# Optimization experiments

Hardware: AMD Instinct MI355X
Metric: run time of the kernel (lower is better)

## Reference

```python
import jax, jax.numpy as jnp
import numpy as np

L = 5          # num_layer
H = 32         # num_heads (feature dim)
G = 32         # n_graph
NN = 256       # n_node per graph
KB = 8         # adjacency band half-width
N = G * (2 * (KB * NN - KB * (KB + 1) // 2))   # 128768 angle-graph nodes
E = N * 16                                      # 2060288 angle-graph edges
NRBF = 20
BN_EPS = 1e-5
GAMMA = 10.0


def _band_adj():
    i = np.arange(NN)
    d = np.abs(i[:, None] - i[None, :])
    a = (d <= KB) & (d > 0)
    return jnp.asarray(np.broadcast_to(a, (G, NN, NN)).copy())


def setup_inputs() -> dict:
    key = jax.random.key(0)
    ks = jax.random.split(key, 10)
    adj = _band_adj()
    x_mask = jnp.ones((G, NN), dtype=bool)
    x_3d = jax.random.uniform(ks[0], (N, 1), minval=0.8, maxval=1.8)
    edge_attr_3d = jax.random.uniform(ks[1], (E, 1), minval=0.0, maxval=float(np.pi))
    edge_index = jax.random.randint(ks[2], (2, E), 0, N)
    s1 = 1.0 / np.sqrt(NRBF)
    sH = 1.0 / np.sqrt(H)
    s2H = 1.0 / np.sqrt(2 * H)
    return {
        "x_3d": x_3d, "edge_attr_3d": edge_attr_3d,
        "edge_index": edge_index, "adj": adj, "x_mask": x_mask,
        "w_len": jax.random.normal(ks[3], (NRBF, H)) * s1, "b_len": jnp.zeros(H),
        "w_ang": jax.random.normal(ks[4], (NRBF, H)) * s1, "b_ang": jnp.zeros(H),
        "w1": jax.random.normal(ks[5], (L, H, 2 * H)) * sH, "b1": jnp.zeros((L, 2 * H)),
        "bn1_g": jnp.ones((L, 2 * H)), "bn1_b": jnp.zeros((L, 2 * H)),
        "w2": jax.random.normal(ks[6], (L, 2 * H, H)) * s2H, "b2": jnp.zeros((L, H)),
        "eps_gin": jnp.zeros(L),
        "bn_g": jnp.ones((L, H)), "bn_b": jnp.zeros((L, H)),
        "ln_g": jnp.ones(H), "ln_b": jnp.zeros(H),
    }


def _bn(h, g, b):
    # BatchNorm1d in training mode (batch statistics)
    m = jnp.mean(h, axis=0)
    v = jnp.var(h, axis=0)
    return (h - m) * jax.lax.rsqrt(v + BN_EPS) * g + b


def _rbf(x, centers):
    # x: [M,1] -> [M, NRBF]
    return jnp.exp(-GAMMA * (x - centers) ** 2)


def _forward(x_3d, edge_attr_3d, edge_index, adj,
             w_len, b_len, w_ang, b_ang,
             w1, b1, bn1_g, bn1_b, w2, b2, eps_gin, bn_g, bn_b, ln_g, ln_b):
    cen_len = jnp.arange(NRBF, dtype=x_3d.dtype) * 0.1           # bond length RBF centers
    cen_ang = jnp.linspace(0.0, np.pi, NRBF).astype(x_3d.dtype)  # bond angle RBF centers
    x = _rbf(x_3d, cen_len) @ w_len + b_len                      # [N,H]
    ea = _rbf(edge_attr_3d, cen_ang) @ w_ang + b_ang             # [E,H]
    src, dst = edge_index[0], edge_index[1]

    h = x
    for l in range(L):
        # GINConvBondAngle: message = relu(x_j + edge_attr); aggr = add
        msg = jax.nn.relu(h[src] + ea)                           # [E,H]
        agg = jax.ops.segment_sum(msg, dst, num_segments=N)      # [N,H]
        z = (1.0 + eps_gin[l]) * h + agg
        z = _bn(z @ w1[l] + b1[l], bn1_g[l], bn1_b[l])           # mlp Linear+BN
        z = jax.nn.relu(z) @ w2[l] + b2[l]                       # mlp ReLU+Linear
        h = _bn(z, bn_g[l], bn_b[l])                             # outer batch norm
        if l != L - 1:
            h = jax.nn.relu(h)
        # dropout p=0 -> identity; residual=False; JK='last'

    mu = jnp.mean(h, axis=-1, keepdims=True)
    var = jnp.var(h, axis=-1, keepdims=True)
    nr = (h - mu) * jax.lax.rsqrt(var + BN_EPS) * ln_g + ln_b    # LayerNorm, [N,H]

    # masked dense scatter into [G*NN*NN, H]
    eye = jnp.eye(NN, dtype=bool)
    mask = (adj & ~eye).reshape(-1)                              # exactly N Trues
    pos = jnp.cumsum(mask) - 1                                   # row in nr for each True
    out = jnp.where(mask[:, None], nr[jnp.clip(pos, 0, N - 1)], 0.0)
    return out.reshape(G, NN, NN, H).transpose(0, 3, 1, 2)       # [G,H,NN,NN]


def reference(x_3d, edge_attr_3d, edge_index, adj, x_mask,
              w_len, b_len, w_ang, b_ang,
              w1, b1, bn1_g, bn1_b, w2, b2, eps_gin, bn_g, bn_b, ln_g, ln_b):
    return _forward(x_3d, edge_attr_3d, edge_index, adj,
                    w_len, b_len, w_ang, b_ang,
                    w1, b1, bn1_g, bn1_b, w2, b2, eps_gin, bn_g, bn_b, ln_g, ln_b)
```

## Files before the change

### kernel.cpp

```cpp
#include <hip/hip_runtime.h>
#include <hip/hip_bf16.h>
#include <hip/hip_fp16.h>

#define HH 32
#define HH2 64
#define NRBF_ 20
#define NL 5
#define NNN 256
#define KBW 8
#define PGN 4024
#define TTAB 4096
constexpr int NNODE = 128768;
constexpr int NEDGE = 2060288;
constexpr float BNEPS = 1e-5f;
constexpr float PI_F = 3.14159265358979323846f;

#define EMB_BLKS (NNODE * HH / 256)
#define TAB_BLKS (TTAB * HH / 256)
#define HIST_BLKS (NEDGE / 256)

__global__ void __launch_bounds__(256) k_prep(const float* __restrict__ x3d,
                                              const float* __restrict__ wlen,
                                              const float* __restrict__ blen,
                                              const float* __restrict__ wang,
                                              const float* __restrict__ bang,
                                              const int* __restrict__ dst,
                                              __half* __restrict__ hbuf,
                                              __half* __restrict__ tab,
                                              int* __restrict__ counts) {
  int b = blockIdx.x;
  int t = threadIdx.x;
  if (b < EMB_BLKS) {
    __shared__ float wl[NRBF_ * HH];
    __shared__ float bl[HH];
    for (int j = t; j < NRBF_ * HH; j += 256) wl[j] = wlen[j];
    if (t < HH) bl[t] = blen[t];
    __syncthreads();
    int idx = b * 256 + t;
    int n = idx >> 5, c = idx & 31;
    float x = x3d[n];
    float acc = bl[c];
#pragma unroll
    for (int k = 0; k < NRBF_; ++k) {
      float d = x - 0.1f * (float)k;
      acc = fmaf(__expf(-10.f * d * d), wl[k * HH + c], acc);
    }
    hbuf[idx] = __float2half(acc);
  } else if (b < EMB_BLKS + TAB_BLKS) {
    __shared__ float wa[NRBF_ * HH];
    __shared__ float ba[HH];
    for (int j = t; j < NRBF_ * HH; j += 256) wa[j] = wang[j];
    if (t < HH) ba[t] = bang[t];
    __syncthreads();
    int idx = (b - EMB_BLKS) * 256 + t;
    int row = idx >> 5, c = idx & 31;
    float ang = (float)row * (PI_F / (float)(TTAB - 1));
    const float step = PI_F / 19.f;
    float acc = ba[c];
#pragma unroll
    for (int k = 0; k < NRBF_; ++k) {
      float d = ang - step * (float)k;
      acc = fmaf(__expf(-10.f * d * d), wa[k * HH + c], acc);
    }
    tab[row * HH + c] = __float2half(acc);
  } else {
    int e = (b - EMB_BLKS - TAB_BLKS) * 256 + t;
    atomicAdd(&counts[dst[e]], 1);
  }
}

__global__ void __launch_bounds__(256) k_scan1(const int* __restrict__ counts, int* __restrict__ bsum) {
  __shared__ int sd[256];
  int t = threadIdx.x;
  sd[t] = counts[blockIdx.x * 256 + t];
  __syncthreads();
  for (int s = 128; s > 0; s >>= 1) { if (t < s) sd[t] += sd[t + s]; __syncthreads(); }
  if (t == 0) bsum[blockIdx.x] = sd[0];
}

__global__ void __launch_bounds__(512) k_scan2(const int* __restrict__ bsum, int* __restrict__ boff) {
  __shared__ int sd[512];
  int t = threadIdx.x;
  int v = (t < 503) ? bsum[t] : 0;
  sd[t] = v;
  __syncthreads();
  for (int off = 1; off < 512; off <<= 1) {
    int x = (t >= off) ? sd[t - off] : 0;
    __syncthreads();
    sd[t] += x;
    __syncthreads();
  }
  if (t < 503) boff[t] = sd[t] - v;
}

__global__ void __launch_bounds__(256) k_scan3(const int* __restrict__ counts, const int* __restrict__ boff,
                                               int* __restrict__ rowptr, int* __restrict__ cursor) {
  __shared__ int sd[256];
  int t = threadIdx.x;
  int i = blockIdx.x * 256 + t;
  int v = counts[i];
  sd[t] = v;
  __syncthreads();
  for (int off = 1; off < 256; off <<= 1) {
    int x = (t >= off) ? sd[t - off] : 0;
    __syncthreads();
    sd[t] += x;
    __syncthreads();
  }
  int excl = sd[t] - v + boff[blockIdx.x];
  rowptr[i] = excl;
  cursor[i] = excl;
  if (i == NNODE - 1) rowptr[NNODE] = excl + v;
}

__global__ void __launch_bounds__(256) k_scatter(const int* __restrict__ srcA,
                                                 const int* __restrict__ dstA,
                                                 const float* __restrict__ eattr,
                                                 int* __restrict__ cursor,
                                                 unsigned int* __restrict__ pk) {
  const float angsc = (float)(TTAB - 1) / PI_F;
  int bid = blockIdx.x;
  int x = bid & 7;
  int j = bid >> 3;
  int lo = x * (NNODE / 8);
  int hi = lo + (NNODE / 8);
  int e0 = j * 2048 + threadIdx.x;
#pragma unroll
  for (int k = 0; k < 8; ++k) {
    int e = e0 + k * 256;
    int d = dstA[e];
    if (d >= lo && d < hi) {
      int pos = atomicAdd(&cursor[d], 1);
      unsigned int idx = min((unsigned int)fmaf(eattr[e], angsc, 0.5f), (unsigned int)(TTAB - 1));
      pk[pos] = (unsigned int)srcA[e] | (idx << 17);
    }
  }
}

__global__ void __launch_bounds__(256) k_layerA(const __half* __restrict__ hbuf,
                                                const int* __restrict__ rowptr,
                                                const unsigned int* __restrict__ pk,
                                                const __half* __restrict__ tab,
                                                const float* __restrict__ statsC,
                                                const float* __restrict__ bng,
                                                const float* __restrict__ bnb,
                                                const float* __restrict__ w1g,
                                                const float* __restrict__ b1g,
                                                const float* __restrict__ epsg,
                                                __half* __restrict__ y1buf,
                                                float* __restrict__ statsA,
                                                int l, int relu) {
  __shared__ float w1s[HH * HH2];
  __shared__ float b1s[HH2];
  __shared__ float affs[HH], affsh[HH];
  __shared__ float tb[32][HH + 1];
  __shared__ float ps[HH2], pq[HH2];
  int t = threadIdx.x;
  const float* w1l = w1g + l * HH * HH2;
  for (int j = t; j < HH * HH2; j += 256) w1s[j] = w1l[j];
  if (t < HH2) { b1s[t] = b1g[l * HH2 + t]; ps[t] = 0.f; pq[t] = 0.f; }
  if (t < HH) {
    if (l == 0) { affs[t] = 1.f; affsh[t] = 0.f; }
    else {
      float sum = statsC[(l - 1) * 64 + t], sq = statsC[(l - 1) * 64 + 32 + t];
      float mean = sum / (float)NNODE;
      float var = fmaxf(sq / (float)NNODE - mean * mean, 0.f);
      float s = bng[(l - 1) * HH + t] * rsqrtf(var + BNEPS);
      affs[t] = s; affsh[t] = bnb[(l - 1) * HH + t] - mean * s;
    }
  }
  int g = t >> 3, c = t & 7;
  int c4 = c * 4, c8 = c * 8;
  float epsv = 1.f + epsg[l];
  float lo = relu ? 0.f : -3.4e38f;
  float sA0 = 0.f, sA1 = 0.f, sA2 = 0.f, sA3 = 0.f, sA4 = 0.f, sA5 = 0.f, sA6 = 0.f, sA7 = 0.f;
  float sQ0 = 0.f, sQ1 = 0.f, sQ2 = 0.f, sQ3 = 0.f, sQ4 = 0.f, sQ5 = 0.f, sQ6 = 0.f, sQ7 = 0.f;
  __syncthreads();
  float sc0 = affs[c4], sh0 = affsh[c4];
  float sc1 = affs[c4 + 1], sh1 = affsh[c4 + 1];
  float sc2 = affs[c4 + 2], sh2 = affsh[c4 + 2];
  float sc3 = affs[c4 + 3], sh3 = affsh[c4 + 3];
  int stride = gridDim.x * 32;
  int iters = (NNODE + stride - 1) / stride;
  int n = blockIdx.x * 32 + g;
  for (int it = 0; it < iters; ++it, n += stride) {
    bool val = n < NNODE;
    if (val) {
      int p0 = rowptr[n], p1 = rowptr[n + 1];
      uint2 HN = *(const uint2*)&hbuf[n * HH + c4];
      float2 hn01 = __half22float2(*(__half2*)&HN.x);
      float2 hn23 = __half22float2(*(__half2*)&HN.y);
      float a0 = 0.f, a1 = 0.f, a2 = 0.f, a3 = 0.f;
      for (int p = p0; p < p1; p += 8) {
        unsigned int qv[8];
        float okf[8];
        uint2 Hv[8], Ev[8];
#pragma unroll
        for (int i = 0; i < 8; ++i) {
          int pi = p + i;
          bool ok = pi < p1;
          okf[i] = ok ? 1.f : 0.f;
          qv[i] = __builtin_nontemporal_load(&pk[ok ? pi : p0]);
        }
#pragma unroll
        for (int i = 0; i < 8; ++i) {
          Hv[i] = *(const uint2*)&hbuf[(qv[i] & 0x1FFFF) * HH + c4];
          Ev[i] = *(const uint2*)&tab[(qv[i] >> 17) * HH + c4];
        }
#pragma unroll
        for (int i = 0; i < 8; ++i) {
          float2 f01 = __half22float2(*(__half2*)&Hv[i].x);
          float2 f23 = __half22float2(*(__half2*)&Hv[i].y);
          float2 e01 = __half22float2(*(__half2*)&Ev[i].x);
          float2 e23 = __half22float2(*(__half2*)&Ev[i].y);
          a0 += okf[i] * fmaxf(fmaxf(fmaf(f01.x, sc0, sh0), lo) + e01.x, 0.f);
          a1 += okf[i] * fmaxf(fmaxf(fmaf(f01.y, sc1, sh1), lo) + e01.y, 0.f);
          a2 += okf[i] * fmaxf(fmaxf(fmaf(f23.x, sc2, sh2), lo) + e23.x, 0.f);
          a3 += okf[i] * fmaxf(fmaxf(fmaf(f23.y, sc3, sh3), lo) + e23.y, 0.f);
        }
      }
      tb[g][c4]     = fmaf(epsv, fmaxf(fmaf(hn01.x, sc0, sh0), lo), a0);
      tb[g][c4 + 1] = fmaf(epsv, fmaxf(fmaf(hn01.y, sc1, sh1), lo), a1);
      tb[g][c4 + 2] = fmaf(epsv, fmaxf(fmaf(hn23.x, sc2, sh2), lo), a2);
      tb[g][c4 + 3] = fmaf(epsv, fmaxf(fmaf(hn23.y, sc3, sh3), lo), a3);
    }
    __builtin_amdgcn_wave_barrier();
    if (val) {
      float y0 = b1s[c8], y1 = b1s[c8 + 1], y2 = b1s[c8 + 2], y3 = b1s[c8 + 3];
      float y4 = b1s[c8 + 4], y5 = b1s[c8 + 5], y6 = b1s[c8 + 6], y7 = b1s[c8 + 7];
#pragma unroll
      for (int k = 0; k < HH; ++k) {
        float tk = tb[g][k];
        const float* wr = &w1s[k * HH2 + c8];
        y0 = fmaf(tk, wr[0], y0); y1 = fmaf(tk, wr[1], y1);
        y2 = fmaf(tk, wr[2], y2); y3 = fmaf(tk, wr[3], y3);
        y4 = fmaf(tk, wr[4], y4); y5 = fmaf(tk, wr[5], y5);
        y6 = fmaf(tk, wr[6], y6); y7 = fmaf(tk, wr[7], y7);
      }
      __half2 h01 = __floats2half2_rn(y0, y1);
      __half2 h23 = __floats2half2_rn(y2, y3);
      __half2 h45 = __floats2half2_rn(y4, y5);
      __half2 h67 = __floats2half2_rn(y6, y7);
      uint4 pack;
      pack.x = *(unsigned int*)&h01; pack.y = *(unsigned int*)&h23;
      pack.z = *(unsigned int*)&h45; pack.w = *(unsigned int*)&h67;
      *(uint4*)&y1buf[n * HH2 + c8] = pack;
      float2 z01 = __half22float2(h01), z23 = __half22float2(h23);
      float2 z45 = __half22float2(h45), z67 = __half22float2(h67);
      sA0 += z01.x; sQ0 += z01.x * z01.x; sA1 += z01.y; sQ1 += z01.y * z01.y;
      sA2 += z23.x; sQ2 += z23.x * z23.x; sA3 += z23.y; sQ3 += z23.y * z23.y;
      sA4 += z45.x; sQ4 += z45.x * z45.x; sA5 += z45.y; sQ5 += z45.y * z45.y;
      sA6 += z67.x; sQ6 += z67.x * z67.x; sA7 += z67.y; sQ7 += z67.y * z67.y;
    }
    __builtin_amdgcn_wave_barrier();
  }
#define RED(v) v += __shfl_xor(v, 8); v += __shfl_xor(v, 16); v += __shfl_xor(v, 32);
  RED(sA0) RED(sA1) RED(sA2) RED(sA3) RED(sA4) RED(sA5) RED(sA6) RED(sA7)
  RED(sQ0) RED(sQ1) RED(sQ2) RED(sQ3) RED(sQ4) RED(sQ5) RED(sQ6) RED(sQ7)
#undef RED
  if ((t & 63) < 8) {
    atomicAdd(&ps[c8], sA0); atomicAdd(&ps[c8 + 1], sA1);
    atomicAdd(&ps[c8 + 2], sA2); atomicAdd(&ps[c8 + 3], sA3);
    atomicAdd(&ps[c8 + 4], sA4); atomicAdd(&ps[c8 + 5], sA5);
    atomicAdd(&ps[c8 + 6], sA6); atomicAdd(&ps[c8 + 7], sA7);
    atomicAdd(&pq[c8], sQ0); atomicAdd(&pq[c8 + 1], sQ1);
    atomicAdd(&pq[c8 + 2], sQ2); atomicAdd(&pq[c8 + 3], sQ3);
    atomicAdd(&pq[c8 + 4], sQ4); atomicAdd(&pq[c8 + 5], sQ5);
    atomicAdd(&pq[c8 + 6], sQ6); atomicAdd(&pq[c8 + 7], sQ7);
  }
  __syncthreads();
  if (t < HH2) {
    atomicAdd(&statsA[l * 128 + t], ps[t]);
    atomicAdd(&statsA[l * 128 + 64 + t], pq[t]);
  }
}

__global__ void __launch_bounds__(256) k_layerC(const __half* __restrict__ y1buf,
                                                const float* __restrict__ statsA,
                                                const float* __restrict__ g1,
                                                const float* __restrict__ bb1,
                                                const float* __restrict__ w2g,
                                                const float* __restrict__ b2g,
                                                __half* __restrict__ hbuf,
                                                float* __restrict__ statsC, int l) {
  __shared__ float w2s[HH2 * HH];
  __shared__ float b2s[HH];
  __shared__ float a1s[HH2], a1sh[HH2];
  __shared__ float ab[32][HH2 + 2];
  __shared__ float ps[HH], pq[HH];
  int t = threadIdx.x;
  const float* w2l = w2g + l * HH2 * HH;
  for (int j = t; j < HH2 * HH; j += 256) w2s[j] = w2l[j];
  if (t < HH) { b2s[t] = b2g[l * HH + t]; ps[t] = 0.f; pq[t] = 0.f; }
  if (t < HH2) {
    float sum = statsA[l * 128 + t], sq = statsA[l * 128 + 64 + t];
    float mean = sum / (float)NNODE;
    float var = fmaxf(sq / (float)NNODE - mean * mean, 0.f);
    float s = g1[l * HH2 + t] * rsqrtf(var + BNEPS);
    a1s[t] = s; a1sh[t] = bb1[l * HH2 + t] - mean * s;
  }
  int g = t >> 3, c = t & 7;
  int c8 = c * 8, c4 = c * 4;
  float sa0 = 0.f, sq0 = 0.f, sa1 = 0.f, sq1 = 0.f;
  float sa2 = 0.f, sq2 = 0.f, sa3 = 0.f, sq3 = 0.f;
  __syncthreads();
  int stride = gridDim.x * 32;
  int iters = (NNODE + stride - 1) / stride;
  int n = blockIdx.x * 32 + g;
  for (int it = 0; it < iters; ++it, n += stride) {
    bool val = n < NNODE;
    if (val) {
      uint4 Y = *(const uint4*)&y1buf[n * HH2 + c8];
      float2 y01 = __half22float2(*(__half2*)&Y.x);
      float2 y23 = __half22float2(*(__half2*)&Y.y);
      float2 y45 = __half22float2(*(__half2*)&Y.z);
      float2 y67 = __half22float2(*(__half2*)&Y.w);
      ab[g][c8]     = fmaxf(fmaf(y01.x, a1s[c8],     a1sh[c8]),     0.f);
      ab[g][c8 + 1] = fmaxf(fmaf(y01.y, a1s[c8 + 1], a1sh[c8 + 1]), 0.f);
      ab[g][c8 + 2] = fmaxf(fmaf(y23.x, a1s[c8 + 2], a1sh[c8 + 2]), 0.f);
      ab[g][c8 + 3] = fmaxf(fmaf(y23.y, a1s[c8 + 3], a1sh[c8 + 3]), 0.f);
      ab[g][c8 + 4] = fmaxf(fmaf(y45.x, a1s[c8 + 4], a1sh[c8 + 4]), 0.f);
      ab[g][c8 + 5] = fmaxf(fmaf(y45.y, a1s[c8 + 5], a1sh[c8 + 5]), 0.f);
      ab[g][c8 + 6] = fmaxf(fmaf(y67.x, a1s[c8 + 6], a1sh[c8 + 6]), 0.f);
      ab[g][c8 + 7] = fmaxf(fmaf(y67.y, a1s[c8 + 7], a1sh[c8 + 7]), 0.f);
    }
    __builtin_amdgcn_wave_barrier();
    if (val) {
      float z0 = b2s[c4], z1 = b2s[c4 + 1], z2 = b2s[c4 + 2], z3 = b2s[c4 + 3];
#pragma unroll
      for (int k = 0; k < HH2; ++k) {
        float ak = ab[g][k];
        const float* wr = &w2s[k * HH + c4];
        z0 = fmaf(ak, wr[0], z0); z1 = fmaf(ak, wr[1], z1);
        z2 = fmaf(ak, wr[2], z2); z3 = fmaf(ak, wr[3], z3);
      }
      __half2 zh01 = __floats2half2_rn(z0, z1);
      __half2 zh23 = __floats2half2_rn(z2, z3);
      uint2 pack;
      pack.x = *(unsigned int*)&zh01; pack.y = *(unsigned int*)&zh23;
      *(uint2*)&hbuf[n * HH + c4] = pack;
      float2 zf01 = __half22float2(zh01), zf23 = __half22float2(zh23);
      sa0 += zf01.x; sq0 += zf01.x * zf01.x;
      sa1 += zf01.y; sq1 += zf01.y * zf01.y;
      sa2 += zf23.x; sq2 += zf23.x * zf23.x;
      sa3 += zf23.y; sq3 += zf23.y * zf23.y;
    }
    __builtin_amdgcn_wave_barrier();
  }
#define RED(v) v += __shfl_xor(v, 8); v += __shfl_xor(v, 16); v += __shfl_xor(v, 32);
  RED(sa0) RED(sa1) RED(sa2) RED(sa3)
  RED(sq0) RED(sq1) RED(sq2) RED(sq3)
#undef RED
  if ((t & 63) < 8) {
    atomicAdd(&ps[c4], sa0); atomicAdd(&ps[c4 + 1], sa1);
    atomicAdd(&ps[c4 + 2], sa2); atomicAdd(&ps[c4 + 3], sa3);
    atomicAdd(&pq[c4], sq0); atomicAdd(&pq[c4 + 1], sq1);
    atomicAdd(&pq[c4 + 2], sq2); atomicAdd(&pq[c4 + 3], sq3);
  }
  __syncthreads();
  if (t < HH) atomicAdd(&statsC[l * 64 + t], ps[t]);
  else if (t < HH2) atomicAdd(&statsC[l * 64 + t], pq[t - HH]);
}

__global__ void __launch_bounds__(256) k_output(const __half* __restrict__ hbuf,
                                                const float* __restrict__ statsC,
                                                const float* __restrict__ bng,
                                                const float* __restrict__ bnb,
                                                const float* __restrict__ lng,
                                                const float* __restrict__ lnb,
                                                float* __restrict__ out) {
  __shared__ float nrb[16 * 33];
  __shared__ float affs[HH], affsh[HH];
  int t = threadIdx.x;
  if (t < HH) {
    float sum = statsC[(NL - 1) * 64 + t], sq = statsC[(NL - 1) * 64 + 32 + t];
    float mean = sum / (float)NNODE;
    float var = fmaxf(sq / (float)NNODE - mean * mean, 0.f);
    float s = bng[(NL - 1) * HH + t] * rsqrtf(var + BNEPS);
    affs[t] = s; affsh[t] = bnb[(NL - 1) * HH + t] - mean * s;
  }
  __syncthreads();
  int gi = blockIdx.x;
  int g = gi >> 8, i = gi & 255;
  int jlo = (i - KBW > 0) ? i - KBW : 0;
  int jhi = (i + KBW < NNN - 1) ? i + KBW : NNN - 1;
  int cnt = jhi - jlo;
  int Ai = (i <= 8) ? i * (i - 1) / 2 : 28 + 8 * (i - 8);
  int Bi = (i <= 248) ? 8 * i : 2012 - (256 - i) * (255 - i) / 2;
  int nb = g * PGN + Ai + Bi;
  int r = t >> 5, c = t & 31;
  float sc = affs[c], sh = affsh[c];
  float lg = lng[c], lb = lnb[c];
  for (int rr = r; rr < cnt; rr += 8) {
    float v = fmaf(__half2float(hbuf[(nb + rr) * HH + c]), sc, sh);
    float s = v;
#pragma unroll
    for (int off = 16; off > 0; off >>= 1) s += __shfl_xor(s, off, 32);
    float mean = s * (1.f / 32.f);
    float d = v - mean;
    float q = d * d;
#pragma unroll
    for (int off = 16; off > 0; off >>= 1) q += __shfl_xor(q, off, 32);
    float var = q * (1.f / 32.f);
    nrb[rr * 33 + c] = d * rsqrtf(var + BNEPS) * lg + lb;
  }
  __syncthreads();
  int j = t;
  bool valid = (j >= jlo) & (j <= jhi) & (j != i);
  int rr = j - jlo - ((j > i) ? 1 : 0);
  rr = (rr < 0) ? 0 : ((rr > 15) ? 15 : rr);
  size_t ob = (((size_t)g * HH) * NNN + i) * NNN + j;
#pragma unroll
  for (int h = 0; h < HH; ++h) {
    float val = valid ? nrb[rr * 33 + h] : 0.f;
    __builtin_nontemporal_store(val, &out[ob + (size_t)h * NNN * NNN]);
  }
}

extern "C" void kernel_launch(void* const* d_in, const int* in_sizes, int n_in,
                              void* d_out, int out_size, void* d_ws, size_t ws_size,
                              hipStream_t stream) {
  (void)in_sizes; (void)n_in;
  const float* x3d   = (const float*)d_in[0];
  const float* eattr = (const float*)d_in[1];
  const int*   eidx  = (const int*)d_in[2];
  const float* wlen = (const float*)d_in[5];
  const float* blen = (const float*)d_in[6];
  const float* wang = (const float*)d_in[7];
  const float* bang = (const float*)d_in[8];
  const float* w1g  = (const float*)d_in[9];
  const float* b1g  = (const float*)d_in[10];
  const float* g1   = (const float*)d_in[11];
  const float* bb1  = (const float*)d_in[12];
  const float* w2g  = (const float*)d_in[13];
  const float* b2g  = (const float*)d_in[14];
  const float* epsg = (const float*)d_in[15];
  const float* bng  = (const float*)d_in[16];
  const float* bnb  = (const float*)d_in[17];
  const float* lng  = (const float*)d_in[18];
  const float* lnb  = (const float*)d_in[19];
  float* out = (float*)d_out;

  char* ws = (char*)d_ws;
  size_t off = 0;
  auto alloc = [&](size_t bytes) {
    void* p = ws + off;
    off += (bytes + 255) & ~(size_t)255;
    return p;
  };
  unsigned int* pk  = (unsigned int*)alloc((size_t)NEDGE * 4);
  int*   rowptr     = (int*)alloc((size_t)(NNODE + 1) * 4);
  int*   counts     = (int*)alloc((size_t)NNODE * 4);
  float* statsA     = (float*)alloc((NL * 128 + NL * 64) * 4);
  float* statsC     = statsA + NL * 128;
  int*   cursor     = (int*)alloc((size_t)NNODE * 4);
  __half* hbuf      = (__half*)alloc((size_t)NNODE * HH * 2);
  __half* y1buf     = (__half*)alloc((size_t)NNODE * HH2 * 2);
  __half* tab       = (__half*)alloc((size_t)TTAB * HH * 2);
  int*   bsum       = (int*)alloc(503 * 4);
  int*   boff       = (int*)alloc(503 * 4);

  if (off > ws_size) {
    hipMemsetAsync(d_out, 0x7F, (size_t)out_size * 4, stream);
    return;
  }

  hipMemsetAsync(counts, 0, (size_t)NNODE * 4 + (NL * 128 + NL * 64) * 4, stream);

  k_prep<<<EMB_BLKS + TAB_BLKS + HIST_BLKS, 256, 0, stream>>>(x3d, wlen, blen, wang, bang,
                                                              eidx + NEDGE, hbuf, tab, counts);
  k_scan1<<<NNODE / 256, 256, 0, stream>>>(counts, bsum);
  k_scan2<<<1, 512, 0, stream>>>(bsum, boff);
  k_scan3<<<NNODE / 256, 256, 0, stream>>>(counts, boff, rowptr, cursor);
  k_scatter<<<8048, 256, 0, stream>>>(eidx, eidx + NEDGE, eattr, cursor, pk);

  for (int l = 0; l < NL; ++l) {
    int relu = l >= 1 ? 1 : 0;
    k_layerA<<<2048, 256, 0, stream>>>(hbuf, rowptr, pk, tab, statsC, bng, bnb,
                                       w1g, b1g, epsg, y1buf, statsA, l, relu);
    k_layerC<<<2048, 256, 0, stream>>>(y1buf, statsA, g1, bb1, w2g, b2g, hbuf, statsC, l);
  }

  k_output<<<NNN * 32, 256, 0, stream>>>(hbuf, statsC, bng, bnb, lng, lnb, out);
}
```

Baseline: 945.7 us.

## Use packed fp16 math, shuffled index loads, and a peeled tail in edge aggregation

The per-edge message loop in the layer-A kernel now computes the affine, ReLU and edge-add in packed half2 arithmetic and accumulates through fdot2 into fp32. Each of the 8 lanes of a node group loads one packed edge index and shares it with the others through a width-8 shuffle, so the eight redundant index loads per lane are gone. Full batches of 8 edges run without masking, and only a peeled tail batch is masked. The intermediate math now runs in fp16, which costs precision, and the non-ReLU lower clamp changes to -60000 to stay inside the half range.

Measured after the change: 930.2 us. No clear change (-1.6%).

```diff
diff --git a/kernel.cpp b/kernel.cpp
--- a/kernel.cpp
+++ b/kernel.cpp
@@ -19,6 +19,28 @@
 #define TAB_BLKS (TTAB * HH / 256)
 #define HIST_BLKS (NEDGE / 256)
 
+typedef _Float16 h2v __attribute__((ext_vector_type(2)));
+
+union U32H2 { unsigned int u; h2v v; };
+
+__device__ __forceinline__ h2v u2h(unsigned int u) { U32H2 x; x.u = u; return x.v; }
+
+__device__ __forceinline__ h2v hmax2v(h2v a, h2v b) {
+#if __has_builtin(__builtin_elementwise_max)
+  return __builtin_elementwise_max(a, b);
+#else
+  h2v r; r.x = a.x > b.x ? a.x : b.x; r.y = a.y > b.y ? a.y : b.y; return r;
+#endif
+}
+
+__device__ __forceinline__ float fdot2f(h2v a, h2v b, float c) {
+#if __has_builtin(__builtin_amdgcn_fdot2)
+  return __builtin_amdgcn_fdot2(a, b, c, false);
+#else
+  return fmaf((float)a.x, (float)b.x, fmaf((float)a.y, (float)b.y, c));
+#endif
+}
+
 __global__ void __launch_bounds__(256) k_prep(const float* __restrict__ x3d,
                                               const float* __restrict__ wlen,
                                               const float* __restrict__ blen,
@@ -134,6 +156,44 @@
       unsigned int idx = min((unsigned int)fmaf(eattr[e], angsc, 0.5f), (unsigned int)(TTAB - 1));
       pk[pos] = (unsigned int)srcA[e] | (idx << 17);
     }
+  }
+}
+
+template<bool MASK>
+__device__ __forceinline__ void edge_batch(const __half* __restrict__ hbuf,
+                                           const __half* __restrict__ tab,
+                                           unsigned int myq, int p, int p1, int c4,
+                                           h2v sc01, h2v sh01,
+                                           h2v sc23, h2v sh23, h2v lo2,
+                                           float& a0, float& a1, float& a2, float& a3) {
+  unsigned int qv[8];
+  uint2 Hv[8], Ev[8];
+#pragma unroll
+  for (int i = 0; i < 8; ++i) qv[i] = (unsigned int)__shfl((int)myq, i, 8);
+#pragma unroll
+  for (int i = 0; i < 8; ++i) {
+    Hv[i] = *(const uint2*)&hbuf[(qv[i] & 0x1FFFF) * HH + c4];
+    Ev[i] = *(const uint2*)&tab[(qv[i] >> 17) * HH + c4];
+  }
+  const h2v selA = {(_Float16)1.f, (_Float16)0.f};
+  const h2v selB = {(_Float16)0.f, (_Float16)1.f};
+  const h2v zz   = {(_Float16)0.f, (_Float16)0.f};
+#pragma unroll
+  for (int i = 0; i < 8; ++i) {
+    h2v mkA = selA, mkB = selB;
+    if (MASK) {
+      bool ok = (p + i) < p1;
+      mkA = ok ? selA : zz;
+      mkB = ok ? selB : zz;
+    }
+    h2v h01 = u2h(Hv[i].x), h23 = u2h(Hv[i].y);
+    h2v e01 = u2h(Ev[i].x), e23 = u2h(Ev[i].y);
+    h2v m01 = hmax2v(hmax2v(h01 * sc01 + sh01, lo2) + e01, zz);
+    h2v m23 = hmax2v(hmax2v(h23 * sc23 + sh23, lo2) + e23, zz);
+    a0 = fdot2f(m01, mkA, a0);
+    a1 = fdot2f(m01, mkB, a1);
+    a2 = fdot2f(m23, mkA, a2);
+    a3 = fdot2f(m23, mkB, a3);
   }
 }
 
@@ -172,14 +232,17 @@
   int g = t >> 3, c = t & 7;
   int c4 = c * 4, c8 = c * 8;
   float epsv = 1.f + epsg[l];
-  float lo = relu ? 0.f : -3.4e38f;
+  float lof = relu ? 0.f : -60000.f;
   float sA0 = 0.f, sA1 = 0.f, sA2 = 0.f, sA3 = 0.f, sA4 = 0.f, sA5 = 0.f, sA6 = 0.f, sA7 = 0.f;
   float sQ0 = 0.f, sQ1 = 0.f, sQ2 = 0.f, sQ3 = 0.f, sQ4 = 0.f, sQ5 = 0.f, sQ6 = 0.f, sQ7 = 0.f;
   __syncthreads();
-  float sc0 = affs[c4], sh0 = affsh[c4];
-  float sc1 = affs[c4 + 1], sh1 = affsh[c4 + 1];
-  float sc2 = affs[c4 + 2], sh2 = affsh[c4 + 2];
-  float sc3 = affs[c4 + 3], sh3 = affsh[c4 + 3];
+  float sc0f = affs[c4], sh0f = affsh[c4];
+  float sc1f = affs[c4 + 1], sh1f = affsh[c4 + 1];
+  float sc2f = affs[c4 + 2], sh2f = affsh[c4 + 2];
+  float sc3f = affs[c4 + 3], sh3f = affsh[c4 + 3];
+  h2v sc01 = {(_Float16)sc0f, (_Float16)sc1f}, sh01 = {(_Float16)sh0f, (_Float16)sh1f};
+  h2v sc23 = {(_Float16)sc2f, (_Float16)sc3f}, sh23 = {(_Float16)sh2f, (_Float16)sh3f};
+  h2v lo2 = {(_Float16)lof, (_Float16)lof};
   int stride = gridDim.x * 32;
   int iters = (NNODE + stride - 1) / stride;
   int n = blockIdx.x * 32 + g;
@@ -191,38 +254,20 @@
       float2 hn01 = __half22float2(*(__half2*)&HN.x);
       float2 hn23 = __half22float2(*(__half2*)&HN.y);
       float a0 = 0.f, a1 = 0.f, a2 = 0.f, a3 = 0.f;
-      for (int p = p0; p < p1; p += 8) {
-        unsigned int qv[8];
-        float okf[8];
-        uint2 Hv[8], Ev[8];
-#pragma unroll
-        for (int i = 0; i < 8; ++i) {
-          int pi = p + i;
-          bool ok = pi < p1;
-          okf[i] = ok ? 1.f : 0.f;
-          qv[i] = __builtin_nontemporal_load(&pk[ok ? pi : p0]);
-        }
-#pragma unroll
-        for (int i = 0; i < 8; ++i) {
-          Hv[i] = *(const uint2*)&hbuf[(qv[i] & 0x1FFFF) * HH + c4];
-          Ev[i] = *(const uint2*)&tab[(qv[i] >> 17) * HH + c4];
-        }
-#pragma unroll
-        for (int i = 0; i < 8; ++i) {
-          float2 f01 = __half22float2(*(__half2*)&Hv[i].x);
-          float2 f23 = __half22float2(*(__half2*)&Hv[i].y);
-          float2 e01 = __half22float2(*(__half2*)&Ev[i].x);
-          float2 e23 = __half22float2(*(__half2*)&Ev[i].y);
-          a0 += okf[i] * fmaxf(fmaxf(fmaf(f01.x, sc0, sh0), lo) + e01.x, 0.f);
-          a1 += okf[i] * fmaxf(fmaxf(fmaf(f01.y, sc1, sh1), lo) + e01.y, 0.f);
-          a2 += okf[i] * fmaxf(fmaxf(fmaf(f23.x, sc2, sh2), lo) + e23.x, 0.f);
-          a3 += okf[i] * fmaxf(fmaxf(fmaf(f23.y, sc3, sh3), lo) + e23.y, 0.f);
-        }
+      int p = p0;
+      for (; p + 8 <= p1; p += 8) {
+        unsigned int myq = __builtin_nontemporal_load(&pk[p + c]);
+        edge_batch<false>(hbuf, tab, myq, p, p1, c4, sc01, sh01, sc23, sh23, lo2, a0, a1, a2, a3);
       }
-      tb[g][c4]     = fmaf(epsv, fmaxf(fmaf(hn01.x, sc0, sh0), lo), a0);
-      tb[g][c4 + 1] = fmaf(epsv, fmaxf(fmaf(hn01.y, sc1, sh1), lo), a1);
-      tb[g][c4 + 2] = fmaf(epsv, fmaxf(fmaf(hn23.x, sc2, sh2), lo), a2);
-      tb[g][c4 + 3] = fmaf(epsv, fmaxf(fmaf(hn23.y, sc3, sh3), lo), a3);
+      if (p < p1) {
+        int pidx = p + c;
+        unsigned int myq = __builtin_nontemporal_load(&pk[pidx < p1 ? pidx : p]);
+        edge_batch<true>(hbuf, tab, myq, p, p1, c4, sc01, sh01, sc23, sh23, lo2, a0, a1, a2, a3);
+      }
+      tb[g][c4]     = fmaf(epsv, fmaxf(fmaf(hn01.x, sc0f, sh0f), lof), a0);
+      tb[g][c4 + 1] = fmaf(epsv, fmaxf(fmaf(hn01.y, sc1f, sh1f), lof), a1);
+      tb[g][c4 + 2] = fmaf(epsv, fmaxf(fmaf(hn23.x, sc2f, sh2f), lof), a2);
+      tb[g][c4 + 3] = fmaf(epsv, fmaxf(fmaf(hn23.y, sc3f, sh3f), lof), a3);
     }
     __builtin_amdgcn_wave_barrier();
     if (val) {
```
